# Kernel optimization log

Hardware: AMD Instinct MI355X
Metric: run time of the kernel (lower is better)

## Reference

```python
import jax, jax.numpy as jnp
import numpy as np

N_LEVELS = 17   # max node_order over all trees (cube depth)
H = 128         # tree_dim
EMB = 128       # emb_dim
VOCAB = 50000


def _build_tree(depth, rng, vocab):
    """Complete binary tree; root is the LAST node (matching h[-1] usage).
    node_order = level (leaves=0, root=depth-1); edge_order = parent level."""
    N = 2 ** depth - 1
    heap = np.arange(N)
    heap_depth = np.floor(np.log2(heap + 1)).astype(np.int64)
    level = depth - 1 - heap_depth          # indexed by heap position
    node_order = level[::-1].copy()         # node id j <-> heap N-1-j
    internal = np.arange((N - 1) // 2)      # heap positions with 2 children
    parents = N - 1 - internal
    c1 = N - 1 - (2 * internal + 1)
    c2 = N - 1 - (2 * internal + 2)
    adj = np.stack([np.concatenate([parents, parents]),
                    np.concatenate([c1, c2])], axis=1)
    edge_order = node_order[adj[:, 0]]
    feats = rng.integers(0, vocab, size=N)
    return (jnp.asarray(feats, jnp.int32), jnp.asarray(node_order, jnp.int32),
            jnp.asarray(adj, jnp.int32), jnp.asarray(edge_order, jnp.int32))


def setup_inputs() -> dict:
    rng = np.random.default_rng(0)
    key = jax.random.key(0)
    ks = jax.random.split(key, 8)
    cf, cno, cadj, ceo = _build_tree(17, rng, VOCAB)
    af, ano, aadj, aeo = _build_tree(12, rng, VOCAB)
    bf, bno, badj, beo = _build_tree(12, rng, VOCAB)
    s = lambda k, shp, fan: (jax.random.normal(k, shp, jnp.float32) / np.sqrt(fan)).astype(jnp.float32)
    return dict(
        cube_features=cf, cube_node_order=cno, cube_adjacency_list=cadj, cube_edge_order=ceo,
        lit_a_features=af, lit_a_node_order=ano, lit_a_adjacency_list=aadj, lit_a_edge_order=aeo,
        lit_b_features=bf, lit_b_node_order=bno, lit_b_adjacency_list=badj, lit_b_edge_order=beo,
        emb=s(ks[0], (VOCAB, EMB), EMB),
        W_iou=s(ks[1], (EMB, 3 * H), EMB), b_iou=jnp.zeros((3 * H,), jnp.float32),
        U_iou=s(ks[2], (H, 3 * H), H),
        W_f=s(ks[3], (EMB, H), EMB), b_f=jnp.zeros((H,), jnp.float32),
        U_f=s(ks[4], (H, H), H),
        fc1_w=s(ks[5], (H, H // 2), H), fc1_b=jnp.zeros((H // 2,), jnp.float32),
        fc2_w=s(ks[6], (H // 2, 3), H // 2), fc2_b=jnp.zeros((3,), jnp.float32))


def _tree_lstm(x, node_order, adj, edge_order, W_iou, b_iou, U_iou, W_f, b_f, U_f):
    """Child-sum TreeLSTM over levels. x: (N, EMB) embedded features."""
    N = x.shape[0]
    parent = adj[:, 0]
    child = adj[:, 1]
    x_iou = x @ W_iou + b_iou   # (N, 3H), precomputed input projections
    x_f = x @ W_f + b_f         # (N, H)
    h0 = jnp.zeros((N, H), x.dtype)
    c0 = jnp.zeros((N, H), x.dtype)

    def step(carry, it):
        h, c = carry
        nmask = (node_order == it)[:, None]            # (N,1) nodes at this level
        emask = (edge_order == it)[:, None].astype(h.dtype)  # (E,1)
        # child-sum of hidden states into parents (only this level's edges)
        h_sum = jax.ops.segment_sum(h[child] * emask, parent, num_segments=N)
        iou = x_iou + h_sum @ U_iou                    # U_iou has no bias -> leaves get W_iou(x)
        i, o, u = jnp.split(iou, 3, axis=1)
        i = jax.nn.sigmoid(i)
        o = jax.nn.sigmoid(o)
        u = jnp.tanh(u)
        # per-edge forget gates, then scatter-add f*c_child into parents
        hU = h @ U_f                                   # (N,H)
        f = jax.nn.sigmoid(x_f[parent] + hU[child])    # (E,H)
        c_sum = jax.ops.segment_sum(f * c[child] * emask, parent, num_segments=N)
        c_new = i * u + c_sum
        h_new = o * jnp.tanh(c_new)
        c = jnp.where(nmask, c_new, c)
        h = jnp.where(nmask, h_new, h)
        return (h, c), None

    (h, c), _ = jax.lax.scan(step, (h0, c0), jnp.arange(N_LEVELS))
    return h, c


def reference(cube_features, cube_node_order, cube_adjacency_list, cube_edge_order,
              lit_a_features, lit_a_node_order, lit_a_adjacency_list, lit_a_edge_order,
              lit_b_features, lit_b_node_order, lit_b_adjacency_list, lit_b_edge_order,
              emb, W_iou, b_iou, U_iou, W_f, b_f, U_f, fc1_w, fc1_b, fc2_w, fc2_b):
    run = lambda f, no, a, eo: _tree_lstm(emb[f], no, a, eo, W_iou, b_iou, U_iou, W_f, b_f, U_f)
    h_c, _ = run(cube_features, cube_node_order, cube_adjacency_list, cube_edge_order)
    h_a, _ = run(lit_a_features, lit_a_node_order, lit_a_adjacency_list, lit_a_edge_order)
    h_b, _ = run(lit_b_features, lit_b_node_order, lit_b_adjacency_list, lit_b_edge_order)
    h_c = h_c[-1]                                  # (H,) root hidden of cube
    fuse_a_b = jnp.outer(h_a[-1], h_b[-1])         # (H,H)
    h = fuse_a_b @ h_c                             # (H,)
    return jax.nn.relu(jax.nn.relu(h @ fc1_w + fc1_b) @ fc2_w + fc2_b)
```

## Files before the change

### kernel.cpp

```cpp
#include <hip/hip_runtime.h>
#include <hip/hip_bf16.h>
#include <math.h>

#define H 128
#define EMBD 128
#define VOCAB 50000

typedef __attribute__((ext_vector_type(8))) short bf16x8;
typedef __attribute__((ext_vector_type(4))) float f32x4;

constexpr int BLOCK = 128;
constexpr int NTOT = 131071 + 4095 + 4095;

__device__ float g_pack[128 * 128 * 8];
__device__ unsigned short g_Biou[384 * 1152];
__device__ unsigned short g_Bf[256 * 1152];
__device__ unsigned short g_Bleaf[384 * 384];
__device__ unsigned short g_embhl[VOCAB * 256];

constexpr int SB_NBT[3] = {12, 8, 4};
constexpr int SB_KOFF[3][12] = {
    {0, 64, 128, 192, 256, 320, 768, 832, 896, 960, 1024, 1088},
    {0, 64, 128, 192, 768, 832, 896, 960},
    {0, 64, 256, 320}
};
constexpr int SB_NPL[3][12] = {
    {2, 2, 2, 2, 2, 2, 1, 1, 1, 1, 1, 1},
    {2, 2, 4, 4, 1, 1, 2, 2},
    {2, 2, 1, 1}
};
constexpr int SB_SEL[3][12][4] = {
    {{0,0},{0,0},{1,2},{1,2},{1,2},{1,2},{0},{0},{1},{1},{1},{1}},
    {{0,0},{0,0},{1,1,2,2},{1,1,2,2},{0},{0},{1,1},{1,1}},
    {{0,0},{0,0},{0},{0}}
};
constexpr int SB_OFF[3][12][4] = {
    {{0,128},{64,192},{0,0},{64,64},{128,128},{192,192},{0},{64},{0},{64},{128},{192}},
    {{0,128},{64,192},{0,128,0,128},{64,192,64,192},{0},{64},{0,128},{64,192}},
    {{0,128},{64,192},{0},{64}}
};

struct TreeSeg { int start, cnt, hcOff, N; };

__device__ __forceinline__ float fast_sig(float x)  { return 1.0f / (1.0f + __expf(-x)); }
__device__ __forceinline__ float fast_tanh(float x) { return 1.0f - 2.0f / (__expf(2.0f * x) + 1.0f); }
__device__ __forceinline__ unsigned short f2bf(float f) {
    unsigned int u = __float_as_uint(f);
    return (unsigned short)((u + 0x7FFFu + ((u >> 16) & 1u)) >> 16);
}
__device__ __forceinline__ float bf2f(unsigned short h) {
    return __uint_as_float(((unsigned int)h) << 16);
}
__device__ __forceinline__ unsigned short bf_split(float v, bool lo) {
    unsigned short hi = f2bf(v);
    return lo ? f2bf(v - bf2f(hi)) : hi;
}

__global__ __launch_bounds__(256)
void pack_all(const float* __restrict__ Wiou, const float* __restrict__ Uiou,
              const float* __restrict__ Wf, const float* __restrict__ Uf,
              const float* __restrict__ emb)
{
    const int R0 = 128 * 128;
    const int R1 = R0 + 384 * 1152;
    const int R2 = R1 + 256 * 1152;
    const int R3 = R2 + 384 * 384;
    const int R4 = R3 + VOCAB * 32;
    int idx = blockIdx.x * 256 + threadIdx.x;
    if (idx < R0) {
        const int k = idx >> 7, j = idx & 127;
        float4 a, b;
        a.x = Wiou[k * 384 + j];
        a.y = Wiou[k * 384 + 128 + j];
        a.z = Wiou[k * 384 + 256 + j];
        a.w = Wf[k * 128 + j];
        b.x = Uiou[k * 384 + j];
        b.y = Uiou[k * 384 + 128 + j];
        b.z = Uiou[k * 384 + 256 + j];
        b.w = Uf[k * 128 + j];
        float4* o = reinterpret_cast<float4*>(g_pack + ((size_t)k * 128 + j) * 8);
        o[0] = a;
        o[1] = b;
    } else if (idx < R1) {
        int r = idx - R0;
        int c = r / 1152, k = r % 1152;
        int kb = k % 384; bool lo = k >= 768;
        float v = (kb < 128) ? Wiou[kb * 384 + c] : Uiou[((kb - 128) & 127) * 384 + c];
        g_Biou[c * 1152 + k] = bf_split(v, lo);
    } else if (idx < R2) {
        int r = idx - R1;
        int c = r / 1152, k = r % 1152;
        int kb = k % 384; bool lo = k >= 768;
        int g = c >> 7, j = c & 127;
        float v;
        if (kb < 128)      v = Wf[kb * 128 + j];
        else if (kb < 256) v = (g == 0) ? Uf[(kb - 128) * 128 + j] : 0.0f;
        else               v = (g == 1) ? Uf[(kb - 256) * 128 + j] : 0.0f;
        g_Bf[c * 1152 + k] = bf_split(v, lo);
    } else if (idx < R3) {
        int r = idx - R2;
        int c = r / 384, k = r % 384;
        int kb = k % 128; bool lo = k >= 256;
        g_Bleaf[c * 384 + k] = bf_split(Wiou[kb * 384 + c], lo);
    } else if (idx < R4) {
        int r = idx - R3;
        const int f = r >> 5, k4 = r & 31;
        float4 v = reinterpret_cast<const float4*>(emb + (size_t)f * 128)[k4];
        const float fv[4] = {v.x, v.y, v.z, v.w};
        ushort4 hi4, lo4;
        unsigned short* hp = reinterpret_cast<unsigned short*>(&hi4);
        unsigned short* lp = reinterpret_cast<unsigned short*>(&lo4);
        #pragma unroll
        for (int t = 0; t < 4; ++t) {
            unsigned short hb = f2bf(fv[t]);
            hp[t] = hb;
            lp[t] = f2bf(fv[t] - bf2f(hb));
        }
        *reinterpret_cast<ushort4*>(g_embhl + (size_t)f * 256 + k4 * 4) = hi4;
        *reinterpret_cast<ushort4*>(g_embhl + (size_t)f * 256 + 128 + k4 * 4) = lo4;
    }
}

template<int NCH, int MODE>
__global__ __launch_bounds__(512, 2)
void gemm_level(const int* __restrict__ feat0, const int* __restrict__ feat1,
                const int* __restrict__ feat2,
                const unsigned short* __restrict__ hhi, const unsigned short* __restrict__ hlo,
                unsigned short* __restrict__ whhi, unsigned short* __restrict__ whlo,
                float* __restrict__ cbuf,
                const float* __restrict__ b_iou, const float* __restrict__ b_f,
                TreeSeg s0, TreeSeg s1, TreeSeg s2, int blocks0, int blocks01)
{
    constexpr int KP   = (MODE == 2) ? 384 : 1152;
    constexpr int NBT  = SB_NBT[MODE];
    constexpr int MAXP = (MODE == 1) ? 4 : 2;
    constexpr int NB   = NCH * 2;
    __shared__ unsigned short Als[MAXP][64 * 64];
    __shared__ unsigned short Bls[NCH * 128 * 64];

    const int bid = blockIdx.x;
    TreeSeg seg; const int* feat; int batch;
    if (bid < blocks0)       { seg = s0; feat = feat0; batch = bid; }
    else if (bid < blocks01) { seg = s1; feat = feat1; batch = bid - blocks0; }
    else                     { seg = s2; feat = feat2; batch = bid - blocks01; }

    const int tid = threadIdx.x;
    const int nbase = seg.start + batch * 64;

    const int arow = tid >> 3, aslot = tid & 7;
    const int agnode = nbase + arow;
    const unsigned short* erow = g_embhl + (size_t)feat[agnode] * 256 + aslot * 8;
    const unsigned short* hrhi = erow;
    const unsigned short* hrlo = erow;
    if (MODE != 2) {
        const size_t hbase = (size_t)(seg.hcOff + 2 * agnode - seg.N - 1) * 128 + aslot * 8;
        hrhi = hhi + hbase;
        hrlo = hlo + hbase;
    }
    const int adst = arow * 64 + ((aslot ^ (arow & 7)) << 3);

    const unsigned short* BT = (MODE == 0) ? g_Bf : ((MODE == 2) ? g_Bleaf : g_Biou);
    const int col0 = tid >> 3, slot = tid & 7;
    const unsigned short* bbase = BT + (size_t)col0 * KP + slot * 8;
    const int bd0 = col0 * 64 + ((slot ^ (col0 & 7)) << 3);

    auto srcPlane = [&](int bkt, int p) -> const unsigned short* {
        const int s = SB_SEL[MODE][bkt][p];
        const unsigned short* base = (s == 0) ? erow : ((s == 1) ? hrhi : hrlo);
        return base + SB_OFF[MODE][bkt][p];
    };

    f32x4 acc[2][NCH][2];
    #pragma unroll
    for (int a = 0; a < 2; ++a)
        #pragma unroll
        for (int b = 0; b < NCH; ++b)
            #pragma unroll
            for (int d = 0; d < 2; ++d) acc[a][b][d] = (f32x4){0.f, 0.f, 0.f, 0.f};

    const int lane = tid & 63;
    const int wv = tid >> 6;
    const int wm = wv >> 2, wn = wv & 3;
    const int l15 = lane & 15, l4 = lane >> 4;

    auto mfma_bkt = [&](int npl) {
        #pragma unroll
        for (int st = 0; st < 2; ++st) {
            const int q = st * 4 + l4;
            bf16x8 bfr[NCH][2];
            #pragma unroll
            for (int ch = 0; ch < NCH; ++ch) {
                #pragma unroll
                for (int fc = 0; fc < 2; ++fc) {
                    const int col = ch * 128 + wn * 32 + fc * 16 + l15;
                    bfr[ch][fc] = *reinterpret_cast<const bf16x8*>(&Bls[col * 64 + ((q ^ (col & 7)) << 3)]);
                }
            }
            #pragma unroll
            for (int p = 0; p < MAXP; ++p) {
                if (p >= npl) continue;
                bf16x8 af[2];
                #pragma unroll
                for (int fm = 0; fm < 2; ++fm) {
                    const int row = wm * 32 + fm * 16 + l15;
                    af[fm] = *reinterpret_cast<const bf16x8*>(&Als[p][row * 64 + ((q ^ (row & 7)) << 3)]);
                }
                #pragma unroll
                for (int ch = 0; ch < NCH; ++ch) {
                    #pragma unroll
                    for (int fc = 0; fc < 2; ++fc) {
                        #pragma unroll
                        for (int fm = 0; fm < 2; ++fm)
                            acc[fm][ch][fc] = __builtin_amdgcn_mfma_f32_16x16x32_bf16(af[fm], bfr[ch][fc], acc[fm][ch][fc], 0, 0, 0);
                    }
                }
            }
        }
    };

    bf16x8 aR[MAXP], bR[NB];
    #pragma unroll
    for (int it = 0; it < NB; ++it)
        bR[it] = *reinterpret_cast<const bf16x8*>(bbase + (size_t)it * 64 * KP + SB_KOFF[MODE][0]);
    #pragma unroll
    for (int p = 0; p < MAXP; ++p)
        if (p < SB_NPL[MODE][0]) aR[p] = *reinterpret_cast<const bf16x8*>(srcPlane(0, p));

    #pragma unroll
    for (int bkt = 0; bkt < NBT; ++bkt) {
        #pragma unroll
        for (int it = 0; it < NB; ++it)
            *reinterpret_cast<bf16x8*>(&Bls[bd0 + it * 64 * 64]) = bR[it];
        #pragma unroll
        for (int p = 0; p < MAXP; ++p)
            if (p < SB_NPL[MODE][bkt]) *reinterpret_cast<bf16x8*>(&Als[p][adst]) = aR[p];
        if (bkt + 1 < NBT) {
            #pragma unroll
            for (int it = 0; it < NB; ++it)
                bR[it] = *reinterpret_cast<const bf16x8*>(bbase + (size_t)it * 64 * KP + SB_KOFF[MODE][bkt + 1]);
            #pragma unroll
            for (int p = 0; p < MAXP; ++p)
                if (p < SB_NPL[MODE][bkt + 1]) aR[p] = *reinterpret_cast<const bf16x8*>(srcPlane(bkt + 1, p));
        }
        __syncthreads();
        mfma_bkt(SB_NPL[MODE][bkt]);
        __syncthreads();
    }

    #pragma unroll
    for (int fc = 0; fc < 2; ++fc) {
        const int j = wn * 32 + fc * 16 + l15;
        float bi = 0.f, bo = 0.f, bu = 0.f, bff = 0.f;
        if (MODE == 0) { bff = b_f[j]; }
        else { bi = b_iou[j]; bo = b_iou[128 + j]; bu = b_iou[256 + j]; }
        #pragma unroll
        for (int fm = 0; fm < 2; ++fm) {
            #pragma unroll
            for (int r = 0; r < 4; ++r) {
                const int row_local = wm * 32 + fm * 16 + l4 * 4 + r;
                const int gnode = nbase + row_local;
                const size_t crow = (size_t)(seg.hcOff + gnode) * 128;
                if constexpr (MODE == 0) {
                    const size_t cbase = (size_t)(seg.hcOff + 2 * gnode - seg.N - 1) * 128;
                    const float fa = fast_sig(acc[fm][0][fc][r] + bff);
                    const float fb = fast_sig(acc[fm][1][fc][r] + bff);
                    cbuf[crow + j] = fa * cbuf[cbase + j] + fb * cbuf[cbase + 128 + j];
                } else {
                    const float iv = fast_sig(acc[fm][0][fc][r] + bi);
                    const float ov = fast_sig(acc[fm][1][fc][r] + bo);
                    const float uv = fast_tanh(acc[fm][NCH - 1][fc][r] + bu);
                    float cn = iv * uv;
                    if (MODE == 1) cn += cbuf[crow + j];
                    cbuf[crow + j] = cn;
                    const float hn = ov * fast_tanh(cn);
                    const unsigned short hi16 = f2bf(hn);
                    whhi[crow + j] = hi16;
                    whlo[crow + j] = f2bf(hn - bf2f(hi16));
                }
            }
        }
    }
}

template<int NP, bool LEAF>
__global__ __launch_bounds__(BLOCK, 2)
void level_kernel(const float* __restrict__ emb,
                  const float* __restrict__ b_iou, const float* __restrict__ b_f,
                  const int* __restrict__ feat0, const int* __restrict__ feat1,
                  const int* __restrict__ feat2,
                  const unsigned short* __restrict__ hhi, const unsigned short* __restrict__ hlo,
                  unsigned short* __restrict__ whhi, unsigned short* __restrict__ whlo,
                  float* __restrict__ cbuf,
                  TreeSeg s0, TreeSeg s1, TreeSeg s2,
                  int blocks0, int blocks01)
{
    __shared__ float xe[NP][EMBD];
    __shared__ float ha[LEAF ? 1 : NP][EMBD];
    __shared__ float hb[LEAF ? 1 : NP][EMBD];

    const int bid = blockIdx.x;
    TreeSeg seg; const int* feat; int batch;
    if (bid < blocks0)       { seg = s0; feat = feat0; batch = bid; }
    else if (bid < blocks01) { seg = s1; feat = feat1; batch = bid - blocks0; }
    else                     { seg = s2; feat = feat2; batch = bid - blocks01; }

    const int tid = threadIdx.x;
    const int nbase = seg.start + batch * NP;
    const int nval  = min(NP, seg.start + seg.cnt - nbase);

    for (int idx = tid; idx < NP * (EMBD / 4); idx += BLOCK) {
        const int n  = idx >> 5;
        const int k4 = idx & 31;
        const int node = nbase + min(n, nval - 1);
        const int f = feat[node];
        float4 v = reinterpret_cast<const float4*>(emb + (size_t)f * EMBD)[k4];
        *reinterpret_cast<float4*>(&xe[n][k4 * 4]) = v;
        if (!LEAF) {
            const int a = 2 * node - seg.N - 1;
            const size_t ra = (size_t)(seg.hcOff + a) * H + k4 * 4;
            ushort4 h4 = *reinterpret_cast<const ushort4*>(hhi + ra);
            ushort4 l4v = *reinterpret_cast<const ushort4*>(hlo + ra);
            float4 va;
            va.x = bf2f(h4.x) + bf2f(l4v.x);
            va.y = bf2f(h4.y) + bf2f(l4v.y);
            va.z = bf2f(h4.z) + bf2f(l4v.z);
            va.w = bf2f(h4.w) + bf2f(l4v.w);
            *reinterpret_cast<float4*>(&ha[n][k4 * 4]) = va;
            ushort4 h4b = *reinterpret_cast<const ushort4*>(hhi + ra + H);
            ushort4 l4b = *reinterpret_cast<const ushort4*>(hlo + ra + H);
            float4 vb;
            vb.x = bf2f(h4b.x) + bf2f(l4b.x);
            vb.y = bf2f(h4b.y) + bf2f(l4b.y);
            vb.z = bf2f(h4b.z) + bf2f(l4b.z);
            vb.w = bf2f(h4b.w) + bf2f(l4b.w);
            *reinterpret_cast<float4*>(&hb[n][k4 * 4]) = vb;
        }
    }
    __syncthreads();

    const int j = tid;
    float ai[NP], ao[NP], au[NP], axf[NP], afa[NP], afb[NP];
    {
        const float bi = b_iou[j];
        const float bo = b_iou[H + j];
        const float bu = b_iou[2 * H + j];
        const float bff = LEAF ? 0.0f : b_f[j];
        #pragma unroll
        for (int n = 0; n < NP; ++n) {
            ai[n] = bi; ao[n] = bo; au[n] = bu;
            axf[n] = bff; afa[n] = 0.0f; afb[n] = 0.0f;
        }
    }

    const float* pkj = g_pack + (size_t)j * 8;

    for (int kk = 0; kk < EMBD / 4; ++kk) {
        float4 wa[4], wb[4];
        #pragma unroll
        for (int r = 0; r < 4; ++r) {
            const float* p = pkj + (size_t)(kk * 4 + r) * 1024;
            wa[r] = *reinterpret_cast<const float4*>(p);
            if (!LEAF) wb[r] = *reinterpret_cast<const float4*>(p + 4);
        }
        #pragma unroll
        for (int n = 0; n < NP; ++n) {
            const float4 xv = *reinterpret_cast<const float4*>(&xe[n][kk * 4]);
            const float xs[4] = {xv.x, xv.y, xv.z, xv.w};
            if (!LEAF) {
                const float4 av = *reinterpret_cast<const float4*>(&ha[n][kk * 4]);
                const float4 bv = *reinterpret_cast<const float4*>(&hb[n][kk * 4]);
                const float as[4] = {av.x, av.y, av.z, av.w};
                const float bs[4] = {bv.x, bv.y, bv.z, bv.w};
                #pragma unroll
                for (int r = 0; r < 4; ++r) {
                    const float hs = as[r] + bs[r];
                    ai[n]  = fmaf(xs[r], wa[r].x, ai[n]);
                    ao[n]  = fmaf(xs[r], wa[r].y, ao[n]);
                    au[n]  = fmaf(xs[r], wa[r].z, au[n]);
                    ai[n]  = fmaf(hs,    wb[r].x, ai[n]);
                    ao[n]  = fmaf(hs,    wb[r].y, ao[n]);
                    au[n]  = fmaf(hs,    wb[r].z, au[n]);
                    axf[n] = fmaf(xs[r], wa[r].w, axf[n]);
                    afa[n] = fmaf(as[r], wb[r].w, afa[n]);
                    afb[n] = fmaf(bs[r], wb[r].w, afb[n]);
                }
            } else {
                #pragma unroll
                for (int r = 0; r < 4; ++r) {
                    ai[n] = fmaf(xs[r], wa[r].x, ai[n]);
                    ao[n] = fmaf(xs[r], wa[r].y, ao[n]);
                    au[n] = fmaf(xs[r], wa[r].z, au[n]);
                }
            }
        }
    }

    #pragma unroll
    for (int n = 0; n < NP; ++n) {
        if (n >= nval) break;
        const int node = nbase + n;
        const float iv = fast_sig(ai[n]);
        const float ov = fast_sig(ao[n]);
        const float uv = fast_tanh(au[n]);
        float cn;
        if (LEAF) {
            cn = iv * uv;
        } else {
            const float fav = fast_sig(axf[n] + afa[n]);
            const float fbv = fast_sig(axf[n] + afb[n]);
            const int a = 2 * node - seg.N - 1;
            const float ca  = cbuf[(size_t)(seg.hcOff + a) * H + j];
            const float cb2 = cbuf[(size_t)(seg.hcOff + a + 1) * H + j];
            cn = fmaf(fav, ca, fmaf(fbv, cb2, iv * uv));
        }
        const float hn = ov * fast_tanh(cn);
        const size_t o = (size_t)(seg.hcOff + node) * H + j;
        cbuf[o] = cn;
        const unsigned short hi16 = f2bf(hn);
        whhi[o] = hi16;
        whlo[o] = f2bf(hn - bf2f(hi16));
    }
}

__global__ __launch_bounds__(128)
void final_kernel(const unsigned short* __restrict__ hhi, const unsigned short* __restrict__ hlo,
                  const float* __restrict__ fc1_w, const float* __restrict__ fc1_b,
                  const float* __restrict__ fc2_w, const float* __restrict__ fc2_b,
                  float* __restrict__ out,
                  int rc, int ra, int rb)
{
    __shared__ float sh[128];
    __shared__ float z1[64];
    __shared__ float dots[2];
    const int tid = threadIdx.x;

    const float hc  = bf2f(hhi[(size_t)rc * H + tid]) + bf2f(hlo[(size_t)rc * H + tid]);
    const float hav = bf2f(hhi[(size_t)ra * H + tid]) + bf2f(hlo[(size_t)ra * H + tid]);
    const float hbv = bf2f(hhi[(size_t)rb * H + tid]) + bf2f(hlo[(size_t)rb * H + tid]);

    float p = hbv * hc;
    #pragma unroll
    for (int o = 32; o > 0; o >>= 1) p += __shfl_down(p, o);
    if ((tid & 63) == 0) dots[tid >> 6] = p;
    __syncthreads();
    const float dot = dots[0] + dots[1];
    sh[tid] = hav * dot;
    __syncthreads();

    if (tid < 64) {
        float z = fc1_b[tid];
        for (int i = 0; i < 128; ++i) z = fmaf(sh[i], fc1_w[i * 64 + tid], z);
        z1[tid] = fmaxf(z, 0.0f);
    }
    __syncthreads();
    if (tid < 3) {
        float z = fc2_b[tid];
        for (int jj = 0; jj < 64; ++jj) z = fmaf(z1[jj], fc2_w[jj * 3 + tid], z);
        out[tid] = fmaxf(z, 0.0f);
    }
}

extern "C" void kernel_launch(void* const* d_in, const int* in_sizes, int n_in,
                              void* d_out, int out_size, void* d_ws, size_t ws_size,
                              hipStream_t stream) {
    const float* emb   = (const float*)d_in[12];
    const float* W_iou = (const float*)d_in[13];
    const float* b_iou = (const float*)d_in[14];
    const float* U_iou = (const float*)d_in[15];
    const float* W_f   = (const float*)d_in[16];
    const float* b_f   = (const float*)d_in[17];
    const float* U_f   = (const float*)d_in[18];
    const float* fc1_w = (const float*)d_in[19];
    const float* fc1_b = (const float*)d_in[20];
    const float* fc2_w = (const float*)d_in[21];
    const float* fc2_b = (const float*)d_in[22];
    const int* feats[3] = { (const int*)d_in[0], (const int*)d_in[4], (const int*)d_in[8] };

    const int D[3] = {17, 12, 12};
    const int N[3] = {131071, 4095, 4095};
    const int off[3] = {0, 131071, 131071 + 4095};

    float* cbuf = (float*)d_ws;
    unsigned short* hhi = (unsigned short*)(cbuf + (size_t)NTOT * 128);
    unsigned short* hlo = hhi + (size_t)NTOT * 128;

    {
        const int total = 128 * 128 + 384 * 1152 + 256 * 1152 + 384 * 384 + VOCAB * 32;
        pack_all<<<(total + 255) / 256, 256, 0, stream>>>(W_iou, U_iou, W_f, U_f, emb);
    }

    auto mkseg = [&](int l, int t) {
        TreeSeg s;
        if (l <= D[t] - 1) {
            s.cnt   = 1 << (D[t] - 1 - l);
            s.start = N[t] - (1 << (D[t] - l)) + 1;
        } else { s.cnt = 0; s.start = 0; }
        s.hcOff = off[t]; s.N = N[t];
        return s;
    };

    {
        TreeSeg s0 = mkseg(0, 0), s1 = mkseg(0, 1), s2 = mkseg(0, 2);
        int b0 = s0.cnt / 64, b1 = s1.cnt / 64, b2 = s2.cnt / 64;
        gemm_level<3, 2><<<b0 + b1 + b2, 512, 0, stream>>>(
            feats[0], feats[1], feats[2], hhi, hlo, hhi, hlo, cbuf,
            b_iou, b_f, s0, s1, s2, b0, b0 + b1);
    }

    for (int l = 1; l <= 3; ++l) {
        TreeSeg s0 = mkseg(l, 0), s1 = mkseg(l, 1), s2 = mkseg(l, 2);
        int b0 = s0.cnt / 64, b1 = s1.cnt / 64, b2 = s2.cnt / 64;
        const int total = b0 + b1 + b2;
        gemm_level<2, 0><<<total, 512, 0, stream>>>(
            feats[0], feats[1], feats[2], hhi, hlo, hhi, hlo, cbuf,
            b_iou, b_f, s0, s1, s2, b0, b0 + b1);
        gemm_level<3, 1><<<total, 512, 0, stream>>>(
            feats[0], feats[1], feats[2], hhi, hlo, hhi, hlo, cbuf,
            b_iou, b_f, s0, s1, s2, b0, b0 + b1);
    }

    for (int l = 4; l < 17; ++l) {
        TreeSeg s[3];
        int total_parents = 0;
        for (int t = 0; t < 3; ++t) { s[t] = mkseg(l, t); total_parents += s[t].cnt; }
        if (total_parents == 0) continue;
        const int NPsel = (total_parents >= 2048) ? 4 : 2;
        int blocks[3];
        for (int t = 0; t < 3; ++t) blocks[t] = (s[t].cnt + NPsel - 1) / NPsel;
        const int total = blocks[0] + blocks[1] + blocks[2];
        if (NPsel == 4) {
            level_kernel<4, false><<<total, BLOCK, 0, stream>>>(
                emb, b_iou, b_f, feats[0], feats[1], feats[2],
                hhi, hlo, hhi, hlo, cbuf,
                s[0], s[1], s[2], blocks[0], blocks[0] + blocks[1]);
        } else {
            level_kernel<2, false><<<total, BLOCK, 0, stream>>>(
                emb, b_iou, b_f, feats[0], feats[1], feats[2],
                hhi, hlo, hhi, hlo, cbuf,
                s[0], s[1], s[2], blocks[0], blocks[0] + blocks[1]);
        }
    }

    const int rc = off[0] + N[0] - 1;
    const int ra = off[1] + N[1] - 1;
    const int rb = off[2] + N[2] - 1;
    final_kernel<<<1, 128, 0, stream>>>(hhi, hlo, fc1_w, fc1_b, fc2_w, fc2_b,
                                        (float*)d_out, rc, ra, rb);
}
```

Baseline: 494.3 us.

## Merge forget-gate and iou GEMMs into one kernel for levels one to three

For tree levels 1-3, the two launches (a forget-gate GEMM writing a partial c, then an iou GEMM that adds to it) become one kernel, gemm_merged. It computes all five gate groups (fa, fb, i, o, u) from a single packed 640x768 weight matrix and does the whole cell update in its epilogue. This removes one launch per level, avoids writing and re-reading the intermediate c buffer, and shares the A-operand loads across all gates. In exchange it uses more shared memory (640 B-columns) and more accumulator registers per thread, which may lower occupancy. Dead template paths (the LEAF variant and the unused MODE branches) are also removed.

```diff
diff --git a/kernel.cpp b/kernel.cpp
--- a/kernel.cpp
+++ b/kernel.cpp
@@ -13,8 +13,7 @@
 constexpr int NTOT = 131071 + 4095 + 4095;
 
 __device__ float g_pack[128 * 128 * 8];
-__device__ unsigned short g_Biou[384 * 1152];
-__device__ unsigned short g_Bf[256 * 1152];
+__device__ unsigned short g_Bm[640 * 768];
 __device__ unsigned short g_Bleaf[384 * 384];
 __device__ unsigned short g_embhl[VOCAB * 256];
 
@@ -40,6 +39,11 @@
     {{0,128},{64,192},{0},{64}}
 };
 
+constexpr int M_KOFF[12] = {0, 64, 128, 192, 256, 320, 384, 448, 512, 576, 640, 704};
+constexpr int M_NPL[12]  = {2, 2, 2, 2, 2, 2, 1, 1, 1, 1, 1, 1};
+constexpr int M_SEL[12][2] = {{0,0},{0,0},{1,2},{1,2},{1,2},{1,2},{0,0},{0,0},{1,1},{1,1},{1,1},{1,1}};
+constexpr int M_OFF[12][2] = {{0,128},{64,192},{0,0},{64,64},{128,128},{192,192},{0,0},{64,0},{0,0},{64,0},{128,0},{192,0}};
+
 struct TreeSeg { int start, cnt, hcOff, N; };
 
 __device__ __forceinline__ float fast_sig(float x)  { return 1.0f / (1.0f + __expf(-x)); }
@@ -62,10 +66,9 @@
               const float* __restrict__ emb)
 {
     const int R0 = 128 * 128;
-    const int R1 = R0 + 384 * 1152;
-    const int R2 = R1 + 256 * 1152;
-    const int R3 = R2 + 384 * 384;
-    const int R4 = R3 + VOCAB * 32;
+    const int R1 = R0 + 640 * 768;
+    const int R2 = R1 + 384 * 384;
+    const int R3 = R2 + VOCAB * 32;
     int idx = blockIdx.x * 256 + threadIdx.x;
     if (idx < R0) {
         const int k = idx >> 7, j = idx & 127;
@@ -83,27 +86,29 @@
         o[1] = b;
     } else if (idx < R1) {
         int r = idx - R0;
-        int c = r / 1152, k = r % 1152;
-        int kb = k % 384; bool lo = k >= 768;
-        float v = (kb < 128) ? Wiou[kb * 384 + c] : Uiou[((kb - 128) & 127) * 384 + c];
-        g_Biou[c * 1152 + k] = bf_split(v, lo);
+        int c = r / 768, k = r % 768;
+        int wn = c / 160, lc = c % 160;
+        int gate = lc >> 5, jj = wn * 32 + (lc & 31);
+        int band = k >> 7, kb = k & 127;
+        bool lo = band >= 3;
+        int bb = band % 3;
+        float v;
+        if (bb == 0) {
+            v = (gate < 2) ? Wf[kb * 128 + jj] : Wiou[kb * 384 + (gate - 2) * 128 + jj];
+        } else {
+            const bool isA = (bb == 1);
+            if (gate == 0)      v = isA ? Uf[kb * 128 + jj] : 0.0f;
+            else if (gate == 1) v = isA ? 0.0f : Uf[kb * 128 + jj];
+            else                v = Uiou[kb * 384 + (gate - 2) * 128 + jj];
+        }
+        g_Bm[c * 768 + k] = bf_split(v, lo);
     } else if (idx < R2) {
         int r = idx - R1;
-        int c = r / 1152, k = r % 1152;
-        int kb = k % 384; bool lo = k >= 768;
-        int g = c >> 7, j = c & 127;
-        float v;
-        if (kb < 128)      v = Wf[kb * 128 + j];
-        else if (kb < 256) v = (g == 0) ? Uf[(kb - 128) * 128 + j] : 0.0f;
-        else               v = (g == 1) ? Uf[(kb - 256) * 128 + j] : 0.0f;
-        g_Bf[c * 1152 + k] = bf_split(v, lo);
-    } else if (idx < R3) {
-        int r = idx - R2;
         int c = r / 384, k = r % 384;
         int kb = k % 128; bool lo = k >= 256;
         g_Bleaf[c * 384 + k] = bf_split(Wiou[kb * 384 + c], lo);
-    } else if (idx < R4) {
-        int r = idx - R3;
+    } else if (idx < R3) {
+        int r = idx - R2;
         const int f = r >> 5, k4 = r & 31;
         float4 v = reinterpret_cast<const float4*>(emb + (size_t)f * 128)[k4];
         const float fv[4] = {v.x, v.y, v.z, v.w};
@@ -125,15 +130,14 @@
 __global__ __launch_bounds__(512, 2)
 void gemm_level(const int* __restrict__ feat0, const int* __restrict__ feat1,
                 const int* __restrict__ feat2,
-                const unsigned short* __restrict__ hhi, const unsigned short* __restrict__ hlo,
                 unsigned short* __restrict__ whhi, unsigned short* __restrict__ whlo,
                 float* __restrict__ cbuf,
-                const float* __restrict__ b_iou, const float* __restrict__ b_f,
+                const float* __restrict__ b_iou,
                 TreeSeg s0, TreeSeg s1, TreeSeg s2, int blocks0, int blocks01)
 {
-    constexpr int KP   = (MODE == 2) ? 384 : 1152;
+    constexpr int KP   = 384;
     constexpr int NBT  = SB_NBT[MODE];
-    constexpr int MAXP = (MODE == 1) ? 4 : 2;
+    constexpr int MAXP = 2;
     constexpr int NB   = NCH * 2;
     __shared__ unsigned short Als[MAXP][64 * 64];
     __shared__ unsigned short Bls[NCH * 128 * 64];
@@ -150,24 +154,14 @@
     const int arow = tid >> 3, aslot = tid & 7;
     const int agnode = nbase + arow;
     const unsigned short* erow = g_embhl + (size_t)feat[agnode] * 256 + aslot * 8;
-    const unsigned short* hrhi = erow;
-    const unsigned short* hrlo = erow;
-    if (MODE != 2) {
-        const size_t hbase = (size_t)(seg.hcOff + 2 * agnode - seg.N - 1) * 128 + aslot * 8;
-        hrhi = hhi + hbase;
-        hrlo = hlo + hbase;
-    }
     const int adst = arow * 64 + ((aslot ^ (arow & 7)) << 3);
 
-    const unsigned short* BT = (MODE == 0) ? g_Bf : ((MODE == 2) ? g_Bleaf : g_Biou);
     const int col0 = tid >> 3, slot = tid & 7;
-    const unsigned short* bbase = BT + (size_t)col0 * KP + slot * 8;
+    const unsigned short* bbase = g_Bleaf + (size_t)col0 * KP + slot * 8;
     const int bd0 = col0 * 64 + ((slot ^ (col0 & 7)) << 3);
 
     auto srcPlane = [&](int bkt, int p) -> const unsigned short* {
-        const int s = SB_SEL[MODE][bkt][p];
-        const unsigned short* base = (s == 0) ? erow : ((s == 1) ? hrhi : hrlo);
-        return base + SB_OFF[MODE][bkt][p];
+        return erow + SB_OFF[MODE][bkt][p];
     };
 
     f32x4 acc[2][NCH][2];
@@ -189,13 +183,12 @@
             const int q = st * 4 + l4;
             bf16x8 bfr[NCH][2];
             #pragma unroll
-            for (int ch = 0; ch < NCH; ++ch) {
+            for (int ch = 0; ch < NCH; ++ch)
                 #pragma unroll
                 for (int fc = 0; fc < 2; ++fc) {
                     const int col = ch * 128 + wn * 32 + fc * 16 + l15;
                     bfr[ch][fc] = *reinterpret_cast<const bf16x8*>(&Bls[col * 64 + ((q ^ (col & 7)) << 3)]);
                 }
-            }
             #pragma unroll
             for (int p = 0; p < MAXP; ++p) {
                 if (p >= npl) continue;
@@ -206,14 +199,12 @@
                     af[fm] = *reinterpret_cast<const bf16x8*>(&Als[p][row * 64 + ((q ^ (row & 7)) << 3)]);
                 }
                 #pragma unroll
-                for (int ch = 0; ch < NCH; ++ch) {
+                for (int ch = 0; ch < NCH; ++ch)
                     #pragma unroll
-                    for (int fc = 0; fc < 2; ++fc) {
+                    for (int fc = 0; fc < 2; ++fc)
                         #pragma unroll
                         for (int fm = 0; fm < 2; ++fm)
                             acc[fm][ch][fc] = __builtin_amdgcn_mfma_f32_16x16x32_bf16(af[fm], bfr[ch][fc], acc[fm][ch][fc], 0, 0, 0);
-                    }
-                }
             }
         }
     };
@@ -250,9 +241,9 @@
     #pragma unroll
     for (int fc = 0; fc < 2; ++fc) {
         const int j = wn * 32 + fc * 16 + l15;
-        float bi = 0.f, bo = 0.f, bu = 0.f, bff = 0.f;
-        if (MODE == 0) { bff = b_f[j]; }
-        else { bi = b_iou[j]; bo = b_iou[128 + j]; bu = b_iou[256 + j]; }
+        const float bi = b_iou[j];
+        const float bo = b_iou[128 + j];
+        const float bu = b_iou[256 + j];
         #pragma unroll
         for (int fm = 0; fm < 2; ++fm) {
             #pragma unroll
@@ -260,29 +251,162 @@
                 const int row_local = wm * 32 + fm * 16 + l4 * 4 + r;
                 const int gnode = nbase + row_local;
                 const size_t crow = (size_t)(seg.hcOff + gnode) * 128;
-                if constexpr (MODE == 0) {
-                    const size_t cbase = (size_t)(seg.hcOff + 2 * gnode - seg.N - 1) * 128;
-                    const float fa = fast_sig(acc[fm][0][fc][r] + bff);
-                    const float fb = fast_sig(acc[fm][1][fc][r] + bff);
-                    cbuf[crow + j] = fa * cbuf[cbase + j] + fb * cbuf[cbase + 128 + j];
-                } else {
-                    const float iv = fast_sig(acc[fm][0][fc][r] + bi);
-                    const float ov = fast_sig(acc[fm][1][fc][r] + bo);
-                    const float uv = fast_tanh(acc[fm][NCH - 1][fc][r] + bu);
-                    float cn = iv * uv;
-                    if (MODE == 1) cn += cbuf[crow + j];
-                    cbuf[crow + j] = cn;
-                    const float hn = ov * fast_tanh(cn);
-                    const unsigned short hi16 = f2bf(hn);
-                    whhi[crow + j] = hi16;
-                    whlo[crow + j] = f2bf(hn - bf2f(hi16));
+                const float iv = fast_sig(acc[fm][0][fc][r] + bi);
+                const float ov = fast_sig(acc[fm][1][fc][r] + bo);
+                const float uv = fast_tanh(acc[fm][2][fc][r] + bu);
+                const float cn = iv * uv;
+                cbuf[crow + j] = cn;
+                const float hn = ov * fast_tanh(cn);
+                const unsigned short hi16 = f2bf(hn);
+                whhi[crow + j] = hi16;
+                whlo[crow + j] = f2bf(hn - bf2f(hi16));
+            }
+        }
+    }
+}
+
+__global__ __launch_bounds__(512, 2)
+void gemm_merged(const int* __restrict__ feat0, const int* __restrict__ feat1,
+                 const int* __restrict__ feat2,
+                 const unsigned short* __restrict__ hhi, const unsigned short* __restrict__ hlo,
+                 unsigned short* __restrict__ whhi, unsigned short* __restrict__ whlo,
+                 float* __restrict__ cbuf,
+                 const float* __restrict__ b_iou, const float* __restrict__ b_f,
+                 TreeSeg s0, TreeSeg s1, TreeSeg s2, int blocks0, int blocks01)
+{
+    constexpr int KP = 768;
+    constexpr int NB = 10;
+    constexpr int NFC = 10;
+    __shared__ unsigned short Als[2][64 * 64];
+    __shared__ unsigned short Bls[640 * 64];
+
+    const int bid = blockIdx.x;
+    TreeSeg seg; const int* feat; int batch;
+    if (bid < blocks0)       { seg = s0; feat = feat0; batch = bid; }
+    else if (bid < blocks01) { seg = s1; feat = feat1; batch = bid - blocks0; }
+    else                     { seg = s2; feat = feat2; batch = bid - blocks01; }
+
+    const int tid = threadIdx.x;
+    const int nbase = seg.start + batch * 64;
+
+    const int arow = tid >> 3, aslot = tid & 7;
+    const int agnode = nbase + arow;
+    const unsigned short* erow = g_embhl + (size_t)feat[agnode] * 256 + aslot * 8;
+    const size_t hbase = (size_t)(seg.hcOff + 2 * agnode - seg.N - 1) * 128 + aslot * 8;
+    const unsigned short* hrhi = hhi + hbase;
+    const unsigned short* hrlo = hlo + hbase;
+    const int adst = arow * 64 + ((aslot ^ (arow & 7)) << 3);
+
+    const int col0 = tid >> 3, slot = tid & 7;
+    const unsigned short* bbase = g_Bm + (size_t)col0 * KP + slot * 8;
+    const int bd0 = col0 * 64 + ((slot ^ (col0 & 7)) << 3);
+
+    auto srcPlane = [&](int bkt, int p) -> const unsigned short* {
+        const int s = M_SEL[bkt][p];
+        const unsigned short* base = (s == 0) ? erow : ((s == 1) ? hrhi : hrlo);
+        return base + M_OFF[bkt][p];
+    };
+
+    f32x4 acc[2][NFC];
+    #pragma unroll
+    for (int a = 0; a < 2; ++a)
+        #pragma unroll
+        for (int b = 0; b < NFC; ++b) acc[a][b] = (f32x4){0.f, 0.f, 0.f, 0.f};
+
+    const int lane = tid & 63;
+    const int wv = tid >> 6;
+    const int wm = wv >> 2, wn = wv & 3;
+    const int l15 = lane & 15, l4 = lane >> 4;
+
+    auto mfma_bkt = [&](int npl) {
+        #pragma unroll
+        for (int st = 0; st < 2; ++st) {
+            const int q = st * 4 + l4;
+            bf16x8 bfr[NFC];
+            #pragma unroll
+            for (int fc = 0; fc < NFC; ++fc) {
+                const int col = wn * 160 + fc * 16 + l15;
+                bfr[fc] = *reinterpret_cast<const bf16x8*>(&Bls[col * 64 + ((q ^ (col & 7)) << 3)]);
+            }
+            #pragma unroll
+            for (int p = 0; p < 2; ++p) {
+                if (p >= npl) continue;
+                bf16x8 af[2];
+                #pragma unroll
+                for (int fm = 0; fm < 2; ++fm) {
+                    const int row = wm * 32 + fm * 16 + l15;
+                    af[fm] = *reinterpret_cast<const bf16x8*>(&Als[p][row * 64 + ((q ^ (row & 7)) << 3)]);
                 }
+                #pragma unroll
+                for (int fc = 0; fc < NFC; ++fc)
+                    #pragma unroll
+                    for (int fm = 0; fm < 2; ++fm)
+                        acc[fm][fc] = __builtin_amdgcn_mfma_f32_16x16x32_bf16(af[fm], bfr[fc], acc[fm][fc], 0, 0, 0);
             }
         }
-    }
-}
-
-template<int NP, bool LEAF>
+    };
+
+    bf16x8 aR[2], bR[NB];
+    #pragma unroll
+    for (int it = 0; it < NB; ++it)
+        bR[it] = *reinterpret_cast<const bf16x8*>(bbase + (size_t)it * 64 * KP + M_KOFF[0]);
+    #pragma unroll
+    for (int p = 0; p < 2; ++p)
+        if (p < M_NPL[0]) aR[p] = *reinterpret_cast<const bf16x8*>(srcPlane(0, p));
+
+    #pragma unroll
+    for (int bkt = 0; bkt < 12; ++bkt) {
+        #pragma unroll
+        for (int it = 0; it < NB; ++it)
+            *reinterpret_cast<bf16x8*>(&Bls[bd0 + it * 64 * 64]) = bR[it];
+        #pragma unroll
+        for (int p = 0; p < 2; ++p)
+            if (p < M_NPL[bkt]) *reinterpret_cast<bf16x8*>(&Als[p][adst]) = aR[p];
+        if (bkt + 1 < 12) {
+            #pragma unroll
+            for (int it = 0; it < NB; ++it)
+                bR[it] = *reinterpret_cast<const bf16x8*>(bbase + (size_t)it * 64 * KP + M_KOFF[bkt + 1]);
+            #pragma unroll
+            for (int p = 0; p < 2; ++p)
+                if (p < M_NPL[bkt + 1]) aR[p] = *reinterpret_cast<const bf16x8*>(srcPlane(bkt + 1, p));
+        }
+        __syncthreads();
+        mfma_bkt(M_NPL[bkt]);
+        __syncthreads();
+    }
+
+    #pragma unroll
+    for (int fcL = 0; fcL < 2; ++fcL) {
+        const int j = wn * 32 + fcL * 16 + l15;
+        const float bi = b_iou[j];
+        const float bo = b_iou[128 + j];
+        const float bu = b_iou[256 + j];
+        const float bff = b_f[j];
+        #pragma unroll
+        for (int fm = 0; fm < 2; ++fm) {
+            #pragma unroll
+            for (int r = 0; r < 4; ++r) {
+                const int row_local = wm * 32 + fm * 16 + l4 * 4 + r;
+                const int gnode = nbase + row_local;
+                const size_t crow = (size_t)(seg.hcOff + gnode) * 128;
+                const size_t cbase = (size_t)(seg.hcOff + 2 * gnode - seg.N - 1) * 128;
+                const float fav = fast_sig(acc[fm][0 + fcL][r] + bff);
+                const float fbv = fast_sig(acc[fm][2 + fcL][r] + bff);
+                const float iv  = fast_sig(acc[fm][4 + fcL][r] + bi);
+                const float ov  = fast_sig(acc[fm][6 + fcL][r] + bo);
+                const float uv  = fast_tanh(acc[fm][8 + fcL][r] + bu);
+                const float cn = fav * cbuf[cbase + j] + fbv * cbuf[cbase + 128 + j] + iv * uv;
+                cbuf[crow + j] = cn;
+                const float hn = ov * fast_tanh(cn);
+                const unsigned short hi16 = f2bf(hn);
+                whhi[crow + j] = hi16;
+                whlo[crow + j] = f2bf(hn - bf2f(hi16));
+            }
+        }
+    }
+}
+
+template<int NP>
 __global__ __launch_bounds__(BLOCK, 2)
 void level_kernel(const float* __restrict__ emb,
                   const float* __restrict__ b_iou, const float* __restrict__ b_f,
@@ -295,8 +419,8 @@
                   int blocks0, int blocks01)
 {
     __shared__ float xe[NP][EMBD];
-    __shared__ float ha[LEAF ? 1 : NP][EMBD];
-    __shared__ float hb[LEAF ? 1 : NP][EMBD];
+    __shared__ float ha[NP][EMBD];
+    __shared__ float hb[NP][EMBD];
 
     const int bid = blockIdx.x;
     TreeSeg seg; const int* feat; int batch;
@@ -315,26 +439,24 @@
         const int f = feat[node];
         float4 v = reinterpret_cast<const float4*>(emb + (size_t)f * EMBD)[k4];
         *reinterpret_cast<float4*>(&xe[n][k4 * 4]) = v;
-        if (!LEAF) {
-            const int a = 2 * node - seg.N - 1;
-            const size_t ra = (size_t)(seg.hcOff + a) * H + k4 * 4;
-            ushort4 h4 = *reinterpret_cast<const ushort4*>(hhi + ra);
-            ushort4 l4v = *reinterpret_cast<const ushort4*>(hlo + ra);
-            float4 va;
-            va.x = bf2f(h4.x) + bf2f(l4v.x);
-            va.y = bf2f(h4.y) + bf2f(l4v.y);
-            va.z = bf2f(h4.z) + bf2f(l4v.z);
-            va.w = bf2f(h4.w) + bf2f(l4v.w);
-            *reinterpret_cast<float4*>(&ha[n][k4 * 4]) = va;
-            ushort4 h4b = *reinterpret_cast<const ushort4*>(hhi + ra + H);
-            ushort4 l4b = *reinterpret_cast<const ushort4*>(hlo + ra + H);
-            float4 vb;
-            vb.x = bf2f(h4b.x) + bf2f(l4b.x);
-            vb.y = bf2f(h4b.y) + bf2f(l4b.y);
-            vb.z = bf2f(h4b.z) + bf2f(l4b.z);
-            vb.w = bf2f(h4b.w) + bf2f(l4b.w);
-            *reinterpret_cast<float4*>(&hb[n][k4 * 4]) = vb;
-        }
+        const int a = 2 * node - seg.N - 1;
+        const size_t ra = (size_t)(seg.hcOff + a) * H + k4 * 4;
+        ushort4 h4 = *reinterpret_cast<const ushort4*>(hhi + ra);
+        ushort4 l4v = *reinterpret_cast<const ushort4*>(hlo + ra);
+        float4 va;
+        va.x = bf2f(h4.x) + bf2f(l4v.x);
+        va.y = bf2f(h4.y) + bf2f(l4v.y);
+        va.z = bf2f(h4.z) + bf2f(l4v.z);
+        va.w = bf2f(h4.w) + bf2f(l4v.w);
+        *reinterpret_cast<float4*>(&ha[n][k4 * 4]) = va;
+        ushort4 h4b = *reinterpret_cast<const ushort4*>(hhi + ra + H);
+        ushort4 l4b = *reinterpret_cast<const ushort4*>(hlo + ra + H);
+        float4 vb;
+        vb.x = bf2f(h4b.x) + bf2f(l4b.x);
+        vb.y = bf2f(h4b.y) + bf2f(l4b.y);
+        vb.z = bf2f(h4b.z) + bf2f(l4b.z);
+        vb.w = bf2f(h4b.w) + bf2f(l4b.w);
+        *reinterpret_cast<float4*>(&hb[n][k4 * 4]) = vb;
     }
     __syncthreads();
 
@@ -344,7 +466,7 @@
         const float bi = b_iou[j];
         const float bo = b_iou[H + j];
         const float bu = b_iou[2 * H + j];
-        const float bff = LEAF ? 0.0f : b_f[j];
+        const float bff = b_f[j];
         #pragma unroll
         for (int n = 0; n < NP; ++n) {
             ai[n] = bi; ao[n] = bo; au[n] = bu;
@@ -360,37 +482,28 @@
         for (int r = 0; r < 4; ++r) {
             const float* p = pkj + (size_t)(kk * 4 + r) * 1024;
             wa[r] = *reinterpret_cast<const float4*>(p);
-            if (!LEAF) wb[r] = *reinterpret_cast<const float4*>(p + 4);
+            wb[r] = *reinterpret_cast<const float4*>(p + 4);
         }
         #pragma unroll
         for (int n = 0; n < NP; ++n) {
             const float4 xv = *reinterpret_cast<const float4*>(&xe[n][kk * 4]);
+            const float4 av = *reinterpret_cast<const float4*>(&ha[n][kk * 4]);
+            const float4 bv = *reinterpret_cast<const float4*>(&hb[n][kk * 4]);
             const float xs[4] = {xv.x, xv.y, xv.z, xv.w};
-            if (!LEAF) {
-                const float4 av = *reinterpret_cast<const float4*>(&ha[n][kk * 4]);
-                const float4 bv = *reinterpret_cast<const float4*>(&hb[n][kk * 4]);
-                const float as[4] = {av.x, av.y, av.z, av.w};
-                const float bs[4] = {bv.x, bv.y, bv.z, bv.w};
-                #pragma unroll
-                for (int r = 0; r < 4; ++r) {
-                    const float hs = as[r] + bs[r];
-                    ai[n]  = fmaf(xs[r], wa[r].x, ai[n]);
-                    ao[n]  = fmaf(xs[r], wa[r].y, ao[n]);
-                    au[n]  = fmaf(xs[r], wa[r].z, au[n]);
-                    ai[n]  = fmaf(hs,    wb[r].x, ai[n]);
-                    ao[n]  = fmaf(hs,    wb[r].y, ao[n]);
-                    au[n]  = fmaf(hs,    wb[r].z, au[n]);
-                    axf[n] = fmaf(xs[r], wa[r].w, axf[n]);
-                    afa[n] = fmaf(as[r], wb[r].w, afa[n]);
-                    afb[n] = fmaf(bs[r], wb[r].w, afb[n]);
-                }
-            } else {
-                #pragma unroll
-                for (int r = 0; r < 4; ++r) {
-                    ai[n] = fmaf(xs[r], wa[r].x, ai[n]);
-                    ao[n] = fmaf(xs[r], wa[r].y, ao[n]);
-                    au[n] = fmaf(xs[r], wa[r].z, au[n]);
-                }
+            const float as[4] = {av.x, av.y, av.z, av.w};
+            const float bs[4] = {bv.x, bv.y, bv.z, bv.w};
+            #pragma unroll
+            for (int r = 0; r < 4; ++r) {
+                const float hs = as[r] + bs[r];
+                ai[n]  = fmaf(xs[r], wa[r].x, ai[n]);
+                ao[n]  = fmaf(xs[r], wa[r].y, ao[n]);
+                au[n]  = fmaf(xs[r], wa[r].z, au[n]);
+                ai[n]  = fmaf(hs,    wb[r].x, ai[n]);
+                ao[n]  = fmaf(hs,    wb[r].y, ao[n]);
+                au[n]  = fmaf(hs,    wb[r].z, au[n]);
+                axf[n] = fmaf(xs[r], wa[r].w, axf[n]);
+                afa[n] = fmaf(as[r], wb[r].w, afa[n]);
+                afb[n] = fmaf(bs[r], wb[r].w, afb[n]);
             }
         }
     }
@@ -402,17 +515,12 @@
         const float iv = fast_sig(ai[n]);
         const float ov = fast_sig(ao[n]);
         const float uv = fast_tanh(au[n]);
-        float cn;
-        if (LEAF) {
-            cn = iv * uv;
-        } else {
-            const float fav = fast_sig(axf[n] + afa[n]);
-            const float fbv = fast_sig(axf[n] + afb[n]);
-            const int a = 2 * node - seg.N - 1;
-            const float ca  = cbuf[(size_t)(seg.hcOff + a) * H + j];
-            const float cb2 = cbuf[(size_t)(seg.hcOff + a + 1) * H + j];
-            cn = fmaf(fav, ca, fmaf(fbv, cb2, iv * uv));
-        }
+        const float fav = fast_sig(axf[n] + afa[n]);
+        const float fbv = fast_sig(axf[n] + afb[n]);
+        const int a = 2 * node - seg.N - 1;
+        const float ca  = cbuf[(size_t)(seg.hcOff + a) * H + j];
+        const float cb2 = cbuf[(size_t)(seg.hcOff + a + 1) * H + j];
+        const float cn = fmaf(fav, ca, fmaf(fbv, cb2, iv * uv));
         const float hn = ov * fast_tanh(cn);
         const size_t o = (size_t)(seg.hcOff + node) * H + j;
         cbuf[o] = cn;
@@ -485,7 +593,7 @@
     unsigned short* hlo = hhi + (size_t)NTOT * 128;
 
     {
-        const int total = 128 * 128 + 384 * 1152 + 256 * 1152 + 384 * 384 + VOCAB * 32;
+        const int total = 128 * 128 + 640 * 768 + 384 * 384 + VOCAB * 32;
         pack_all<<<(total + 255) / 256, 256, 0, stream>>>(W_iou, U_iou, W_f, U_f, emb);
     }
 
@@ -503,18 +611,14 @@
         TreeSeg s0 = mkseg(0, 0), s1 = mkseg(0, 1), s2 = mkseg(0, 2);
         int b0 = s0.cnt / 64, b1 = s1.cnt / 64, b2 = s2.cnt / 64;
         gemm_level<3, 2><<<b0 + b1 + b2, 512, 0, stream>>>(
-            feats[0], feats[1], feats[2], hhi, hlo, hhi, hlo, cbuf,
-            b_iou, b_f, s0, s1, s2, b0, b0 + b1);
+            feats[0], feats[1], feats[2], hhi, hlo, cbuf,
+            b_iou, s0, s1, s2, b0, b0 + b1);
     }
 
     for (int l = 1; l <= 3; ++l) {
         TreeSeg s0 = mkseg(l, 0), s1 = mkseg(l, 1), s2 = mkseg(l, 2);
         int b0 = s0.cnt / 64, b1 = s1.cnt / 64, b2 = s2.cnt / 64;
-        const int total = b0 + b1 + b2;
-        gemm_level<2, 0><<<total, 512, 0, stream>>>(
-            feats[0], feats[1], feats[2], hhi, hlo, hhi, hlo, cbuf,
-            b_iou, b_f, s0, s1, s2, b0, b0 + b1);
-        gemm_level<3, 1><<<total, 512, 0, stream>>>(
+        gemm_merged<<<b0 + b1 + b2, 512, 0, stream>>>(
             feats[0], feats[1], feats[2], hhi, hlo, hhi, hlo, cbuf,
             b_iou, b_f, s0, s1, s2, b0, b0 + b1);
     }
@@ -529,12 +633,12 @@
         for (int t = 0; t < 3; ++t) blocks[t] = (s[t].cnt + NPsel - 1) / NPsel;
         const int total = blocks[0] + blocks[1] + blocks[2];
         if (NPsel == 4) {
-            level_kernel<4, false><<<total, BLOCK, 0, stream>>>(
+            level_kernel<4><<<total, BLOCK, 0, stream>>>(
                 emb, b_iou, b_f, feats[0], feats[1], feats[2],
                 hhi, hlo, hhi, hlo, cbuf,
                 s[0], s[1], s[2], blocks[0], blocks[0] + blocks[1]);
         } else {
-            level_kernel<2, false><<<total, BLOCK, 0, stream>>>(
+            level_kernel<2><<<total, BLOCK, 0, stream>>>(
                 emb, b_iou, b_f, feats[0], feats[1], feats[2],
                 hhi, hlo, hhi, hlo, cbuf,
                 s[0], s[1], s[2], blocks[0], blocks[0] + blocks[1]);
```

Result: slower. 520.4 us (+5.3%).
